# Kernel optimization log

Hardware: AMD Instinct MI355X
Metric: run time of the kernel (lower is better)

## Reference

```python
import jax, jax.numpy as jnp
import numpy as np

N_NODES = 100000
N_EDGES = 1600000
F_IN = 128
F_OUT = 128


def _spmm(edge_row, edge_col, edge_weight, X):
    # sparse [N,N] @ dense [N,F]: gather source rows, weight, scatter-add to dest rows
    msgs = edge_weight[:, None] * X[edge_col]  # [E, F]
    return jax.ops.segment_sum(msgs, edge_row, num_segments=N_NODES)


def setup_inputs() -> dict:
    key = jax.random.key(0)
    ks = jax.random.split(key, 7)
    scale = 1.0 / np.sqrt(F_IN)
    return {
        "x": jax.random.normal(ks[0], (N_NODES, F_IN), dtype=jnp.float32),
        "edge_row": jax.random.randint(ks[1], (N_EDGES,), 0, N_NODES, dtype=jnp.int32),
        "edge_col": jax.random.randint(ks[2], (N_EDGES,), 0, N_NODES, dtype=jnp.int32),
        "edge_weight": jax.random.uniform(ks[3], (N_EDGES,), dtype=jnp.float32),
        "w1": jax.random.normal(ks[4], (F_IN, F_IN), dtype=jnp.float32) * scale,
        "w2": jax.random.normal(ks[5], (F_IN, F_OUT), dtype=jnp.float32) * scale,
        "w3": jax.random.normal(ks[6], (F_OUT, F_OUT), dtype=jnp.float32) * scale,
    }


def reference(x, edge_row, edge_col, edge_weight, w1, w2, w3):
    # dropout p=0.0 (eval) -> identity
    h = jax.nn.relu(_spmm(edge_row, edge_col, edge_weight, x @ w1))
    h = jax.nn.relu(_spmm(edge_row, edge_col, edge_weight, h @ w2))
    h = jax.nn.relu(_spmm(edge_row, edge_col, edge_weight, h @ w3))
    return h
```

## Files before the change

### kernel.cpp

```cpp
#include <hip/hip_runtime.h>

#define N_NODES 100000
#define N_EDGES 1600000
#define F 128

#define SCAN_B 1024
#define SCAN_NB ((N_NODES + SCAN_B - 1) / SCAN_B)

typedef short bf16x8 __attribute__((ext_vector_type(8)));
typedef float f32x4  __attribute__((ext_vector_type(4)));

union ABFrag {
    bf16x8 v;
    unsigned short u[8];
    uint4  q;
};

__device__ __forceinline__ unsigned short f2bf(float f) {
    unsigned int u = __float_as_uint(f);
    u += 0x7fffu + ((u >> 16) & 1u);
    return (unsigned short)(u >> 16);
}
__device__ __forceinline__ float bflo(unsigned int u) {
    return __uint_as_float(u << 16);
}
__device__ __forceinline__ float bfhi(unsigned int u) {
    return __uint_as_float(u & 0xFFFF0000u);
}


__global__ void edge_histogram(const int* __restrict__ erow, int* __restrict__ counts) {
    const int e = blockIdx.x * blockDim.x + threadIdx.x;
    atomicAdd(&counts[erow[e]], 1);
}

__global__ void scan_block_sums(const int* __restrict__ counts, int* __restrict__ bsums) {
    __shared__ int s[SCAN_B];
    const int t = threadIdx.x;
    const int idx = blockIdx.x * SCAN_B + t;
    int v = (idx < N_NODES) ? counts[idx] : 0;
    s[t] = v;
    __syncthreads();
    for (int off = SCAN_B / 2; off > 0; off >>= 1) {
        if (t < off) s[t] += s[t + off];
        __syncthreads();
    }
    if (t == 0) bsums[blockIdx.x] = s[0];
}

__global__ void scan_bsums(const int* __restrict__ bsums, int* __restrict__ boffs) {
    __shared__ int s[128];
    const int t = threadIdx.x;
    int v = (t < SCAN_NB) ? bsums[t] : 0;
    s[t] = v;
    __syncthreads();
    for (int off = 1; off < 128; off <<= 1) {
        int u = (t >= off) ? s[t - off] : 0;
        __syncthreads();
        s[t] += u;
        __syncthreads();
    }
    if (t < SCAN_NB) boffs[t] = s[t] - v;
}

__global__ void scan_final(const int* __restrict__ counts, const int* __restrict__ boffs,
                           int* __restrict__ row_ptr) {
    __shared__ int s[SCAN_B];
    const int t = threadIdx.x;
    const int idx = blockIdx.x * SCAN_B + t;
    int v = (idx < N_NODES) ? counts[idx] : 0;
    s[t] = v;
    __syncthreads();
    for (int off = 1; off < SCAN_B; off <<= 1) {
        int u = (t >= off) ? s[t - off] : 0;
        __syncthreads();
        s[t] += u;
        __syncthreads();
    }
    if (idx < N_NODES) row_ptr[idx] = boffs[blockIdx.x] + s[t] - v;
    if (idx == 0) row_ptr[N_NODES] = N_EDGES;
}

__global__ void csr_fill(const int* __restrict__ erow, const int* __restrict__ ecol,
                         const float* __restrict__ ewgt,
                         const int* __restrict__ row_ptr, int* __restrict__ cursor,
                         unsigned int* __restrict__ pairs) {
    const int e = blockIdx.x * blockDim.x + threadIdx.x;
    const int dst = erow[e];
    const int pos = atomicAdd(&cursor[dst], 1);
    pairs[row_ptr[dst] + pos] = ((unsigned int)ecol[e] << 15) | (unsigned int)f2bf(ewgt[e]);
}

__global__ void transpose_w_bf16(const float* __restrict__ W, unsigned short* __restrict__ Wt) {
    const int i = blockIdx.x * 256 + threadIdx.x;
    const int n = i >> 7;
    const int k = i & 127;
    Wt[i] = f2bf(W[k * F + n]);
}

__global__ __launch_bounds__(256) void gemm_mfma(
    const float* __restrict__ Xf,
    const unsigned short* __restrict__ Xb,
    const unsigned short* __restrict__ Wt,
    unsigned short* __restrict__ Y,
    int use_f32_in)
{
    __shared__ unsigned short Wl[4 * 8 * 64 * 8];

    const int tid  = threadIdx.x;
    const int wave = tid >> 6;
    const int lane = tid & 63;

    for (int s = tid; s < 2048; s += 256) {
        const int ln  = s & 63;
        const int ntk = s >> 6;
        const int nt  = ntk & 7;
        const int kt  = ntk >> 3;
        const int n   = nt * 16 + (ln & 15);
        const int k   = kt * 32 + (ln >> 4) * 8;
        *(uint4*)(&Wl[s * 8]) = *(const uint4*)(Wt + n * F + k);
    }
    __syncthreads();

    const int m     = blockIdx.x * 64 + wave * 16 + (lane & 15);
    const bool mval = (m < N_NODES);
    const int kq    = (lane >> 4) * 8;

    f32x4 acc[8] = {};

#pragma unroll
    for (int kt = 0; kt < 4; ++kt) {
        ABFrag a;
        if (mval) {
            if (use_f32_in) {
                const float* p = Xf + (size_t)m * F + kt * 32 + kq;
                const float4 u0 = *(const float4*)p;
                const float4 u1 = *(const float4*)(p + 4);
                a.u[0] = f2bf(u0.x); a.u[1] = f2bf(u0.y);
                a.u[2] = f2bf(u0.z); a.u[3] = f2bf(u0.w);
                a.u[4] = f2bf(u1.x); a.u[5] = f2bf(u1.y);
                a.u[6] = f2bf(u1.z); a.u[7] = f2bf(u1.w);
            } else {
                a.q = *(const uint4*)(Xb + (size_t)m * F + kt * 32 + kq);
#pragma unroll
                for (int j = 0; j < 8; ++j)
                    if (a.u[j] & 0x8000u) a.u[j] = 0;
            }
        } else {
            a.q = make_uint4(0, 0, 0, 0);
        }
#pragma unroll
        for (int nt = 0; nt < 8; ++nt) {
            ABFrag b;
            b.q = *(const uint4*)(&Wl[((kt * 8 + nt) * 64 + lane) * 8]);
            acc[nt] = __builtin_amdgcn_mfma_f32_16x16x32_bf16(a.v, b.v, acc[nt], 0, 0, 0);
        }
    }

    const int rbase = blockIdx.x * 64 + wave * 16 + (lane >> 4) * 4;
    const int cbase = lane & 15;
#pragma unroll
    for (int r = 0; r < 4; ++r) {
        const int row = rbase + r;
        if (row < N_NODES) {
#pragma unroll
            for (int nt = 0; nt < 8; ++nt) {
                Y[(size_t)row * F + nt * 16 + cbase] = f2bf(acc[nt][r]);
            }
        }
    }
}

__global__ __launch_bounds__(256) void spmm_csr_bf16(
    const unsigned short* __restrict__ Xb,
    const int* __restrict__ row_ptr,
    const unsigned int* __restrict__ pairs,
    unsigned short* __restrict__ Ob,
    float* __restrict__ Of,
    int final_mode) {
    const int tid = threadIdx.x;
    const int l16 = tid & 15;
    const int q   = tid >> 4;
    const int row = blockIdx.x * 16 + q;

    const int beg = row_ptr[row];
    const int end = row_ptr[row + 1];

    float a[8] = {};
    int i = beg;
    for (; i + 1 < end; i += 2) {
        const unsigned int p0 = pairs[i], p1 = pairs[i + 1];
        const uint4 v0 = *(const uint4*)(Xb + (size_t)(p0 >> 15) * F + l16 * 8);
        const uint4 v1 = *(const uint4*)(Xb + (size_t)(p1 >> 15) * F + l16 * 8);
        const float w0 = bflo(p0 & 0x7FFFu);
        const float w1 = bflo(p1 & 0x7FFFu);
        a[0] += w0 * bflo(v0.x); a[1] += w0 * bfhi(v0.x);
        a[2] += w0 * bflo(v0.y); a[3] += w0 * bfhi(v0.y);
        a[4] += w0 * bflo(v0.z); a[5] += w0 * bfhi(v0.z);
        a[6] += w0 * bflo(v0.w); a[7] += w0 * bfhi(v0.w);
        a[0] += w1 * bflo(v1.x); a[1] += w1 * bfhi(v1.x);
        a[2] += w1 * bflo(v1.y); a[3] += w1 * bfhi(v1.y);
        a[4] += w1 * bflo(v1.z); a[5] += w1 * bfhi(v1.z);
        a[6] += w1 * bflo(v1.w); a[7] += w1 * bfhi(v1.w);
    }
    if (i < end) {
        const unsigned int p0 = pairs[i];
        const uint4 v0 = *(const uint4*)(Xb + (size_t)(p0 >> 15) * F + l16 * 8);
        const float w0 = bflo(p0 & 0x7FFFu);
        a[0] += w0 * bflo(v0.x); a[1] += w0 * bfhi(v0.x);
        a[2] += w0 * bflo(v0.y); a[3] += w0 * bfhi(v0.y);
        a[4] += w0 * bflo(v0.z); a[5] += w0 * bfhi(v0.z);
        a[6] += w0 * bflo(v0.w); a[7] += w0 * bfhi(v0.w);
    }

    if (final_mode) {
        float4 o0 = {fmaxf(a[0], 0.f), fmaxf(a[1], 0.f), fmaxf(a[2], 0.f), fmaxf(a[3], 0.f)};
        float4 o1 = {fmaxf(a[4], 0.f), fmaxf(a[5], 0.f), fmaxf(a[6], 0.f), fmaxf(a[7], 0.f)};
        float* p = Of + (size_t)row * F + l16 * 8;
        *(float4*)p = o0;
        *(float4*)(p + 4) = o1;
    } else {
        uint4 o;
        o.x = (unsigned int)f2bf(a[0]) | ((unsigned int)f2bf(a[1]) << 16);
        o.y = (unsigned int)f2bf(a[2]) | ((unsigned int)f2bf(a[3]) << 16);
        o.z = (unsigned int)f2bf(a[4]) | ((unsigned int)f2bf(a[5]) << 16);
        o.w = (unsigned int)f2bf(a[6]) | ((unsigned int)f2bf(a[7]) << 16);
        *(uint4*)(Ob + (size_t)row * F + l16 * 8) = o;
    }
}


extern "C" void kernel_launch(void* const* d_in, const int* in_sizes, int n_in,
                              void* d_out, int out_size, void* d_ws, size_t ws_size,
                              hipStream_t stream) {
    const float* x    = (const float*)d_in[0];
    const int*   erow = (const int*)d_in[1];
    const int*   ecol = (const int*)d_in[2];
    const float* ew   = (const float*)d_in[3];
    const float* w1   = (const float*)d_in[4];
    const float* w2   = (const float*)d_in[5];
    const float* w3   = (const float*)d_in[6];
    float* out = (float*)d_out;

    char* ws = (char*)d_ws;
    size_t off = 0;
    auto alloc = [&](size_t bytes) -> char* {
        char* p = ws + off;
        off += (bytes + 255) & ~(size_t)255;
        return p;
    };
    unsigned short* bufA = (unsigned short*)alloc((size_t)N_NODES * F * 2);
    unsigned short* bufB = (unsigned short*)alloc((size_t)N_NODES * F * 2);
    unsigned int* pairs  = (unsigned int*)alloc((size_t)N_EDGES * 4);
    int* counts  = (int*)alloc((size_t)N_NODES * sizeof(int));
    int* row_ptr = (int*)alloc(((size_t)N_NODES + 1) * sizeof(int));
    int* bsums   = (int*)alloc((size_t)SCAN_NB * sizeof(int));
    int* boffs   = (int*)alloc((size_t)SCAN_NB * sizeof(int));
    unsigned short* wt1 = (unsigned short*)alloc((size_t)F * F * 2);
    unsigned short* wt2 = (unsigned short*)alloc((size_t)F * F * 2);
    unsigned short* wt3 = (unsigned short*)alloc((size_t)F * F * 2);

    hipMemsetAsync(counts, 0, (size_t)N_NODES * sizeof(int), stream);
    edge_histogram<<<N_EDGES / 256, 256, 0, stream>>>(erow, counts);
    scan_block_sums<<<SCAN_NB, SCAN_B, 0, stream>>>(counts, bsums);
    scan_bsums<<<1, 128, 0, stream>>>(bsums, boffs);
    scan_final<<<SCAN_NB, SCAN_B, 0, stream>>>(counts, boffs, row_ptr);
    hipMemsetAsync(counts, 0, (size_t)N_NODES * sizeof(int), stream);
    csr_fill<<<N_EDGES / 256, 256, 0, stream>>>(erow, ecol, ew, row_ptr, counts, pairs);

    transpose_w_bf16<<<64, 256, 0, stream>>>(w1, wt1);
    transpose_w_bf16<<<64, 256, 0, stream>>>(w2, wt2);
    transpose_w_bf16<<<64, 256, 0, stream>>>(w3, wt3);

    const int ggrid = (N_NODES + 63) / 64;
    const int sgrid = N_NODES / 16;

    gemm_mfma<<<ggrid, 256, 0, stream>>>(x, nullptr, wt1, bufA, 1);
    spmm_csr_bf16<<<sgrid, 256, 0, stream>>>(bufA, row_ptr, pairs, bufB, nullptr, 0);
    gemm_mfma<<<ggrid, 256, 0, stream>>>(nullptr, bufB, wt2, bufA, 0);
    spmm_csr_bf16<<<sgrid, 256, 0, stream>>>(bufA, row_ptr, pairs, bufB, nullptr, 0);
    gemm_mfma<<<ggrid, 256, 0, stream>>>(nullptr, bufB, wt3, bufA, 0);
    spmm_csr_bf16<<<sgrid, 256, 0, stream>>>(bufA, row_ptr, pairs, nullptr, out, 1);
}
```

Before: 506.3 us.

## Split SpMM into column slices with edge-parallel lanes and shuffle reduction

The SpMM kernel now launches 8 blocks per row chunk, each covering a 16-column slice. Within a row, 8 lanes process different edges in parallel, each fetching 16 bytes per edge, and a cross-lane xor shuffle reduces the partial sums. Edge-pair loads are marked nontemporal, and the second memset is removed by giving csr_fill its own zeroed cursor array. The aim is more memory-level parallelism on short rows and a smaller per-block working set of X columns. The cost is eight reads of row_ptr and pairs per row, a shuffle reduction, and only one lane in eight doing the store.

```diff
diff --git a/kernel.cpp b/kernel.cpp
--- a/kernel.cpp
+++ b/kernel.cpp
@@ -171,27 +171,32 @@
     }
 }
 
-__global__ __launch_bounds__(256) void spmm_csr_bf16(
+__global__ __launch_bounds__(256) void spmm_sliced(
     const unsigned short* __restrict__ Xb,
     const int* __restrict__ row_ptr,
     const unsigned int* __restrict__ pairs,
     unsigned short* __restrict__ Ob,
     float* __restrict__ Of,
     int final_mode) {
-    const int tid = threadIdx.x;
-    const int l16 = tid & 15;
-    const int q   = tid >> 4;
-    const int row = blockIdx.x * 16 + q;
+    const int tid    = threadIdx.x;
+    const int slice  = blockIdx.x & 7;
+    const int chunk  = blockIdx.x >> 3;
+    const int row    = chunk * 16 + (tid >> 4);
+    const int l16    = tid & 15;
+    const int epos   = l16 >> 1;
+    const int par    = l16 & 1;
+    const int colOff = slice * 16 + par * 8;
 
     const int beg = row_ptr[row];
     const int end = row_ptr[row + 1];
 
     float a[8] = {};
-    int i = beg;
-    for (; i + 1 < end; i += 2) {
-        const unsigned int p0 = pairs[i], p1 = pairs[i + 1];
-        const uint4 v0 = *(const uint4*)(Xb + (size_t)(p0 >> 15) * F + l16 * 8);
-        const uint4 v1 = *(const uint4*)(Xb + (size_t)(p1 >> 15) * F + l16 * 8);
+    int i = beg + epos;
+    for (; i + 8 < end; i += 16) {
+        const unsigned int p0 = __builtin_nontemporal_load(&pairs[i]);
+        const unsigned int p1 = __builtin_nontemporal_load(&pairs[i + 8]);
+        const uint4 v0 = *(const uint4*)(Xb + (size_t)(p0 >> 15) * F + colOff);
+        const uint4 v1 = *(const uint4*)(Xb + (size_t)(p1 >> 15) * F + colOff);
         const float w0 = bflo(p0 & 0x7FFFu);
         const float w1 = bflo(p1 & 0x7FFFu);
         a[0] += w0 * bflo(v0.x); a[1] += w0 * bfhi(v0.x);
@@ -204,8 +209,8 @@
         a[6] += w1 * bflo(v1.w); a[7] += w1 * bfhi(v1.w);
     }
     if (i < end) {
-        const unsigned int p0 = pairs[i];
-        const uint4 v0 = *(const uint4*)(Xb + (size_t)(p0 >> 15) * F + l16 * 8);
+        const unsigned int p0 = __builtin_nontemporal_load(&pairs[i]);
+        const uint4 v0 = *(const uint4*)(Xb + (size_t)(p0 >> 15) * F + colOff);
         const float w0 = bflo(p0 & 0x7FFFu);
         a[0] += w0 * bflo(v0.x); a[1] += w0 * bfhi(v0.x);
         a[2] += w0 * bflo(v0.y); a[3] += w0 * bfhi(v0.y);
@@ -213,19 +218,27 @@
         a[6] += w0 * bflo(v0.w); a[7] += w0 * bfhi(v0.w);
     }
 
-    if (final_mode) {
-        float4 o0 = {fmaxf(a[0], 0.f), fmaxf(a[1], 0.f), fmaxf(a[2], 0.f), fmaxf(a[3], 0.f)};
-        float4 o1 = {fmaxf(a[4], 0.f), fmaxf(a[5], 0.f), fmaxf(a[6], 0.f), fmaxf(a[7], 0.f)};
-        float* p = Of + (size_t)row * F + l16 * 8;
-        *(float4*)p = o0;
-        *(float4*)(p + 4) = o1;
-    } else {
-        uint4 o;
-        o.x = (unsigned int)f2bf(a[0]) | ((unsigned int)f2bf(a[1]) << 16);
-        o.y = (unsigned int)f2bf(a[2]) | ((unsigned int)f2bf(a[3]) << 16);
-        o.z = (unsigned int)f2bf(a[4]) | ((unsigned int)f2bf(a[5]) << 16);
-        o.w = (unsigned int)f2bf(a[6]) | ((unsigned int)f2bf(a[7]) << 16);
-        *(uint4*)(Ob + (size_t)row * F + l16 * 8) = o;
+#pragma unroll
+    for (int s = 2; s <= 8; s <<= 1) {
+#pragma unroll
+        for (int j = 0; j < 8; ++j) a[j] += __shfl_xor(a[j], s);
+    }
+
+    if (epos == 0) {
+        if (final_mode) {
+            float* p = Of + (size_t)row * F + colOff;
+            float4 o0 = {fmaxf(a[0], 0.f), fmaxf(a[1], 0.f), fmaxf(a[2], 0.f), fmaxf(a[3], 0.f)};
+            float4 o1 = {fmaxf(a[4], 0.f), fmaxf(a[5], 0.f), fmaxf(a[6], 0.f), fmaxf(a[7], 0.f)};
+            *(float4*)p = o0;
+            *(float4*)(p + 4) = o1;
+        } else {
+            uint4 o;
+            o.x = (unsigned int)f2bf(a[0]) | ((unsigned int)f2bf(a[1]) << 16);
+            o.y = (unsigned int)f2bf(a[2]) | ((unsigned int)f2bf(a[3]) << 16);
+            o.z = (unsigned int)f2bf(a[4]) | ((unsigned int)f2bf(a[5]) << 16);
+            o.w = (unsigned int)f2bf(a[6]) | ((unsigned int)f2bf(a[7]) << 16);
+            *(uint4*)(Ob + (size_t)row * F + colOff) = o;
+        }
     }
 }
 
@@ -252,7 +265,8 @@
     unsigned short* bufA = (unsigned short*)alloc((size_t)N_NODES * F * 2);
     unsigned short* bufB = (unsigned short*)alloc((size_t)N_NODES * F * 2);
     unsigned int* pairs  = (unsigned int*)alloc((size_t)N_EDGES * 4);
-    int* counts  = (int*)alloc((size_t)N_NODES * sizeof(int));
+    int* counts  = (int*)alloc((size_t)N_NODES * sizeof(int) * 2);
+    int* cursor  = counts + N_NODES;
     int* row_ptr = (int*)alloc(((size_t)N_NODES + 1) * sizeof(int));
     int* bsums   = (int*)alloc((size_t)SCAN_NB * sizeof(int));
     int* boffs   = (int*)alloc((size_t)SCAN_NB * sizeof(int));
@@ -260,25 +274,24 @@
     unsigned short* wt2 = (unsigned short*)alloc((size_t)F * F * 2);
     unsigned short* wt3 = (unsigned short*)alloc((size_t)F * F * 2);
 
-    hipMemsetAsync(counts, 0, (size_t)N_NODES * sizeof(int), stream);
+    hipMemsetAsync(counts, 0, (size_t)N_NODES * sizeof(int) * 2, stream);
     edge_histogram<<<N_EDGES / 256, 256, 0, stream>>>(erow, counts);
     scan_block_sums<<<SCAN_NB, SCAN_B, 0, stream>>>(counts, bsums);
     scan_bsums<<<1, 128, 0, stream>>>(bsums, boffs);
     scan_final<<<SCAN_NB, SCAN_B, 0, stream>>>(counts, boffs, row_ptr);
-    hipMemsetAsync(counts, 0, (size_t)N_NODES * sizeof(int), stream);
-    csr_fill<<<N_EDGES / 256, 256, 0, stream>>>(erow, ecol, ew, row_ptr, counts, pairs);
+    csr_fill<<<N_EDGES / 256, 256, 0, stream>>>(erow, ecol, ew, row_ptr, cursor, pairs);
 
     transpose_w_bf16<<<64, 256, 0, stream>>>(w1, wt1);
     transpose_w_bf16<<<64, 256, 0, stream>>>(w2, wt2);
     transpose_w_bf16<<<64, 256, 0, stream>>>(w3, wt3);
 
     const int ggrid = (N_NODES + 63) / 64;
-    const int sgrid = N_NODES / 16;
+    const int sgrid = 8 * (N_NODES / 16);
 
     gemm_mfma<<<ggrid, 256, 0, stream>>>(x, nullptr, wt1, bufA, 1);
-    spmm_csr_bf16<<<sgrid, 256, 0, stream>>>(bufA, row_ptr, pairs, bufB, nullptr, 0);
+    spmm_sliced<<<sgrid, 256, 0, stream>>>(bufA, row_ptr, pairs, bufB, nullptr, 0);
     gemm_mfma<<<ggrid, 256, 0, stream>>>(nullptr, bufB, wt2, bufA, 0);
-    spmm_csr_bf16<<<sgrid, 256, 0, stream>>>(bufA, row_ptr, pairs, bufB, nullptr, 0);
+    spmm_sliced<<<sgrid, 256, 0, stream>>>(bufA, row_ptr, pairs, bufB, nullptr, 0);
     gemm_mfma<<<ggrid, 256, 0, stream>>>(nullptr, bufB, wt3, bufA, 0);
-    spmm_csr_bf16<<<sgrid, 256, 0, stream>>>(bufA, row_ptr, pairs, nullptr, out, 1);
-}
+    spmm_sliced<<<sgrid, 256, 0, stream>>>(bufA, row_ptr, pairs, nullptr, out, 1);
+}
```

New measurement: 856.3 us. 1.69x slower.
